# Optimization experiments

Hardware: AMD Instinct MI355X
Metric: run time of the kernel (lower is better)

Reference implementation:

```python
import jax, jax.numpy as jnp
import numpy as np

RNN_HID = 64
INPUT_DIM = 35
SEQ_LEN = 48
BATCH = 4096


def setup_inputs() -> dict:
    key = jax.random.key(0)
    ks = jax.random.split(key, 16)
    x_t = jax.random.normal(ks[0], (BATCH, SEQ_LEN, INPUT_DIM), jnp.float32)
    masks = (jax.random.uniform(ks[1], (BATCH, SEQ_LEN, INPUT_DIM)) > 0.2).astype(jnp.float32)
    deltas = jax.random.uniform(ks[2], (BATCH, SEQ_LEN, INPUT_DIM), jnp.float32)
    evals = jax.random.normal(ks[3], (BATCH, SEQ_LEN, INPUT_DIM), jnp.float32)
    eval_masks = (jax.random.uniform(ks[4], (BATCH, SEQ_LEN, INPUT_DIM)) > 0.8).astype(jnp.float32)
    is_train = jnp.ones((BATCH,), jnp.float32)

    in_sz = INPUT_DIM * 2  # LSTMCell input = concat(x_c, m)
    s_lstm = 1.0 / np.sqrt(RNN_HID)
    # torch LSTMCell params: W_ih [4H, in], W_hh [4H, H], b_ih [4H], b_hh [4H]
    W_ih = jax.random.uniform(ks[5], (4 * RNN_HID, in_sz), jnp.float32, -s_lstm, s_lstm)
    W_hh = jax.random.uniform(ks[6], (4 * RNN_HID, RNN_HID), jnp.float32, -s_lstm, s_lstm)
    b_ih = jax.random.uniform(ks[7], (4 * RNN_HID,), jnp.float32, -s_lstm, s_lstm)
    b_hh = jax.random.uniform(ks[8], (4 * RNN_HID,), jnp.float32, -s_lstm, s_lstm)
    W_reg = jax.random.uniform(ks[9], (INPUT_DIM, RNN_HID), jnp.float32, -s_lstm, s_lstm)
    b_reg = jax.random.uniform(ks[10], (INPUT_DIM,), jnp.float32, -s_lstm, s_lstm)
    # TemporalDecay: W [RNN_HID, input_dim], b [RNN_HID]
    W_td = jax.random.uniform(ks[11], (RNN_HID, INPUT_DIM), jnp.float32, -s_lstm, s_lstm)
    b_td = jax.random.uniform(ks[12], (RNN_HID,), jnp.float32, -s_lstm, s_lstm)
    # out Linear(RNN_HID -> 1)
    W_out = jax.random.uniform(ks[13], (1, RNN_HID), jnp.float32, -s_lstm, s_lstm)
    b_out = jax.random.uniform(ks[14], (1,), jnp.float32, -s_lstm, s_lstm)
    return {
        'x_t': x_t, 'masks': masks, 'deltas': deltas, 'evals': evals,
        'eval_masks': eval_masks, 'is_train': is_train,
        'W_ih': W_ih, 'W_hh': W_hh, 'b_ih': b_ih, 'b_hh': b_hh,
        'W_reg': W_reg, 'b_reg': b_reg, 'W_td': W_td, 'b_td': b_td,
        'W_out': W_out, 'b_out': b_out,
    }


def _lstm_cell(inp, h, c, W_ih, W_hh, b_ih, b_hh):
    # gates ordered i, f, g, o as in torch.nn.LSTMCell
    gates = inp @ W_ih.T + h @ W_hh.T + b_ih + b_hh  # [B, 4H]
    i, f, g, o = jnp.split(gates, 4, axis=-1)
    i = jax.nn.sigmoid(i)
    f = jax.nn.sigmoid(f)
    g = jnp.tanh(g)
    o = jax.nn.sigmoid(o)
    c_new = f * c + i * g
    h_new = o * jnp.tanh(c_new)
    return h_new, c_new


def reference(x_t, masks, deltas, evals, eval_masks, is_train,
              W_ih, W_hh, b_ih, b_hh, W_reg, b_reg, W_td, b_td, W_out, b_out):
    B, T, D = x_t.shape
    h0 = jnp.zeros((B, RNN_HID), x_t.dtype)
    c0 = jnp.zeros((B, RNN_HID), x_t.dtype)

    def step(carry, xs):
        h, c, x_loss = carry
        x, m, d = xs  # each [B, D]
        x_hat = h @ W_reg.T + b_reg
        x_c = m * x + (1.0 - m) * x_hat
        x_loss = x_loss + jnp.sum(jnp.abs(x - x_hat) * m) / (jnp.sum(m) + 1e-5)
        inputs = jnp.concatenate([x_c, m], axis=1)  # [B, 2D]
        # temporal decay (computed as in original, result unused)
        gamma = jnp.exp(-jax.nn.relu(d @ W_td.T + b_td))
        h, c = _lstm_cell(inputs, h, c, W_ih, W_hh, b_ih, b_hh)
        return (h, c, x_loss), x_c

    xs = (jnp.swapaxes(x_t, 0, 1), jnp.swapaxes(masks, 0, 1), jnp.swapaxes(deltas, 0, 1))
    (h, c, x_loss), imp = jax.lax.scan(step, (h0, c0, jnp.float32(0.0)), xs)
    imputations = jnp.swapaxes(imp, 0, 1)  # [B, T, D]
    y_h = jax.nn.sigmoid(h @ W_out.T + b_out)
    loss = x_loss / T  # y_loss == 0
    return loss, y_h, imputations
```

## Files before the change

kernel.cpp:

```cpp
#include <hip/hip_runtime.h>
#include <stdint.h>

#define B_    4096
#define T_    48
#define D_    35
#define KROW  168
#define ROWEL (T_ * D_)
#define L2E   1.44269504f

typedef float f32x4 __attribute__((ext_vector_type(4)));
typedef short bf16x8 __attribute__((ext_vector_type(8)));

static __device__ __forceinline__ uint32_t fbits(float x){union{float f;uint32_t u;}v;v.f=x;return v.u;}
static __device__ __forceinline__ float bitsf(uint32_t u){union{uint32_t u;float f;}v;v.u=u;return v.f;}
static __device__ __forceinline__ float bf2f(uint32_t b){return bitsf(b<<16);}
static __device__ __forceinline__ unsigned short f2bf_rne(float x){
    uint32_t u=fbits(x); return (unsigned short)((u+0x7fffu+((u>>16)&1u))>>16);
}
static __device__ __forceinline__ float rcp_(float x){return __builtin_amdgcn_rcpf(x);}
static __device__ __forceinline__ float exp2_(float x){return __builtin_amdgcn_exp2f(x);}
#define MFMA __builtin_amdgcn_mfma_f32_16x16x32_bf16

static __device__ __forceinline__ void step_barrier() {
    asm volatile("s_waitcnt lgkmcnt(0)" ::: "memory");
    __builtin_amdgcn_s_barrier();
    __builtin_amdgcn_sched_barrier(0);
}


__global__ __launch_bounds__(512, 1)
void brits_main(const float* __restrict__ x_t, const float* __restrict__ masks,
                const float* __restrict__ W_ih, const float* __restrict__ W_hh,
                const float* __restrict__ b_ih, const float* __restrict__ b_hh,
                const float* __restrict__ W_reg, const float* __restrict__ b_reg,
                const float* __restrict__ W_out, const float* __restrict__ b_out,
                float* __restrict__ ws, float* __restrict__ out)
{
    __shared__ __align__(16) unsigned short Abuf[2][16 * KROW];
    __shared__ __align__(16) unsigned short stash[16 * ROWEL];
    __shared__ unsigned long long mbits[16 * T_];
    __shared__ float lsum[T_ * 3 * 64];
    __shared__ float wout[65];

    const int tid    = threadIdx.x;
    const int lane   = tid & 63;
    const int w      = tid >> 6;
    const int g      = lane >> 4;
    const int cc     = lane & 15;
    const int batch0 = blockIdx.x * 16;
    const int u      = (w & 3) * 16 + cc;
    const int u2     = (w - 4) * 16 + cc;

    for (int i = tid; i < 16 * KROW; i += 512) ((uint32_t*)Abuf)[i] = 0;
    if (tid < 65) wout[tid] = (tid < 64) ? W_out[tid] : b_out[0];

    for (int i = tid; i < 16 * 210; i += 512) {
        const int r = i / 210;
        const int o = (i - r * 210) * 8;
        const float* xp = x_t   + (size_t)(batch0 + r) * ROWEL + o;
        const float* mp = masks + (size_t)(batch0 + r) * ROWEL + o;
        float xv[8], mv[8];
        *(float4*)&xv[0] = *(const float4*)xp; *(float4*)&xv[4] = *(const float4*)(xp + 4);
        *(float4*)&mv[0] = *(const float4*)mp; *(float4*)&mv[4] = *(const float4*)(mp + 4);
        unsigned short pk[8];
        #pragma unroll
        for (int k = 0; k < 8; ++k) pk[k] = f2bf_rne(mv[k] * xv[k]);
        *(uint4*)&stash[r * ROWEL + o] = *(const uint4*)pk;
    }
    for (int p = tid; p < 16 * T_; p += 512) {
        const int r = p / T_, t = p - r * T_;
        const float* mp = masks + (size_t)(batch0 + r) * ROWEL + t * D_;
        unsigned long long bits = 0;
        for (int d = 0; d < D_; ++d) bits |= (unsigned long long)(mp[d] != 0.f) << d;
        mbits[p] = bits;
    }

    bf16x8 Wf[4][5];
    float bIs = 0.f, bFs = 0.f, bGs = 0.f, bOs = 0.f;
    if (w < 4) {
        #pragma unroll
        for (int G = 0; G < 4; ++G) {
            const int n = G * 64 + u;
            #pragma unroll
            for (int kc = 0; kc < 5; ++kc) {
                bf16x8 v;
                #pragma unroll
                for (int i = 0; i < 8; ++i) {
                    const int k = kc * 32 + 8 * g + i;
                    float f = 0.f;
                    if (k < 70)                  f = W_ih[n * 70 + k];
                    else if (k >= 72 && k < 136) f = W_hh[n * 64 + (k - 72)];
                    v[i] = (short)f2bf_rne(f);
                }
                Wf[G][kc] = v;
            }
        }
        bIs = -(b_ih[u]       + b_hh[u])       * L2E;
        bFs = -(b_ih[64 + u]  + b_hh[64 + u])  * L2E;
        bGs = -(b_ih[128 + u] + b_hh[128 + u]) * 2.f * L2E;
        bOs = -(b_ih[192 + u] + b_hh[192 + u]) * L2E;
    }
    bf16x8 Wr0 = {0,0,0,0,0,0,0,0}, Wr1 = {0,0,0,0,0,0,0,0};
    float brg = 0.f;
    const bool pw = (w >= 4) && (w < 7);
    const bool pl = pw && (u2 < 35);
    if (pl) {
        #pragma unroll
        for (int i = 0; i < 8; ++i) {
            Wr0[i] = (short)f2bf_rne(W_reg[u2 * 64 + 8 * g + i]);
            Wr1[i] = (short)f2bf_rne(W_reg[u2 * 64 + 32 + 8 * g + i]);
        }
        brg = b_reg[u2];
    }
    __syncthreads();

    unsigned long long PM[4] = {0, 0, 0, 0};
    uint32_t xmr[4] = {0, 0, 0, 0};
    float* orow[4];
    if (pl) {
        #pragma unroll
        for (int j = 0; j < 4; ++j) {
            const int row = 4 * g + j;
            unsigned long long pm = 0;
            for (int t = 0; t < T_; ++t)
                pm |= ((mbits[row * T_ + t] >> u2) & 1ull) << t;
            PM[j] = pm;
            xmr[j] = stash[row * ROWEL + u2];
            Abuf[0][row * KROW + 35 + u2] = (pm & 1ull) ? (unsigned short)0x3F80 : (unsigned short)0;
            orow[j] = out + 1 + B_ + (size_t)(batch0 + row) * ROWEL + u2;
        }
    }
    __syncthreads();

    float c_[4] = {0.f, 0.f, 0.f, 0.f};

    for (int t = 0; t < T_; ++t) {
        unsigned short* A  = Abuf[t & 1];
        unsigned short* An = Abuf[(t + 1) & 1];

        f32x4 gIa = {0,0,0,0}, gFa = {0,0,0,0}, gGa = {0,0,0,0}, gOa = {0,0,0,0};
        f32x4 gIb = {0,0,0,0}, gFb = {0,0,0,0}, gGb = {0,0,0,0}, gOb = {0,0,0,0};

        if (w < 4) {
            bf16x8 a2 = *(const bf16x8*)&A[cc * KROW + 64  + 8 * g];
            bf16x8 a3 = *(const bf16x8*)&A[cc * KROW + 96  + 8 * g];
            bf16x8 a4 = *(const bf16x8*)&A[cc * KROW + 128 + 8 * g];
            gIa = MFMA(a2, Wf[0][2], gIa, 0,0,0);
            gFa = MFMA(a2, Wf[1][2], gFa, 0,0,0);
            gGa = MFMA(a2, Wf[2][2], gGa, 0,0,0);
            gOa = MFMA(a2, Wf[3][2], gOa, 0,0,0);
            gIb = MFMA(a3, Wf[0][3], gIb, 0,0,0);
            gFb = MFMA(a3, Wf[1][3], gFb, 0,0,0);
            gGb = MFMA(a3, Wf[2][3], gGb, 0,0,0);
            gOb = MFMA(a3, Wf[3][3], gOb, 0,0,0);
            gIa = MFMA(a4, Wf[0][4], gIa, 0,0,0);
            gFa = MFMA(a4, Wf[1][4], gFa, 0,0,0);
            gGa = MFMA(a4, Wf[2][4], gGa, 0,0,0);
            gOa = MFMA(a4, Wf[3][4], gOa, 0,0,0);
        } else if (pw) {
            bf16x8 ah0 = *(const bf16x8*)&A[cc * KROW + 72  + 8 * g];
            bf16x8 ah1 = *(const bf16x8*)&A[cc * KROW + 104 + 8 * g];
            f32x4 p0 = {0,0,0,0};
            p0 = MFMA(ah0, Wr0, p0, 0,0,0);
            p0 = MFMA(ah1, Wr1, p0, 0,0,0);
            float lnum = 0.f;
            if (pl) {
                #pragma unroll
                for (int j = 0; j < 4; ++j) {
                    const int row = 4 * g + j;
                    const float xh = p0[j] + brg;
                    const float xm = bf2f(xmr[j]);
                    const uint32_t mb = (uint32_t)(PM[j] >> t) & 1u;
                    lnum += mb ? fabsf(xm - xh) : 0.f;
                    const unsigned short xc16 = mb ? (unsigned short)xmr[j] : f2bf_rne(xh);
                    A[row * KROW + u2] = xc16;
                    An[row * KROW + 35 + u2] =
                        ((PM[j] >> (t + 1)) & 1ull) ? (unsigned short)0x3F80 : (unsigned short)0;
                    orow[j][t * D_] = bf2f((uint32_t)xc16);
                }
            }
            lsum[(t * 3 + (w - 4)) * 64 + lane] = lnum;
        }
        step_barrier();

        if (w < 4) {
            bf16x8 a0 = *(const bf16x8*)&A[cc * KROW + 0  + 8 * g];
            bf16x8 a1 = *(const bf16x8*)&A[cc * KROW + 32 + 8 * g];
            gIa = MFMA(a0, Wf[0][0], gIa, 0,0,0);
            gFa = MFMA(a0, Wf[1][0], gFa, 0,0,0);
            gGa = MFMA(a0, Wf[2][0], gGa, 0,0,0);
            gOa = MFMA(a0, Wf[3][0], gOa, 0,0,0);
            gIb = MFMA(a1, Wf[0][1], gIb, 0,0,0);
            gFb = MFMA(a1, Wf[1][1], gFb, 0,0,0);
            gGb = MFMA(a1, Wf[2][1], gGb, 0,0,0);
            gOb = MFMA(a1, Wf[3][1], gOb, 0,0,0);
            const f32x4 gI = gIa + gIb;
            const f32x4 gF = gFa + gFb;
            const f32x4 gG = gGa + gGb;
            const f32x4 gO = gOa + gOb;
            #pragma unroll
            for (int j = 0; j < 4; ++j) {
                const float iv = rcp_(1.f + exp2_(fmaf(gI[j], -L2E,       bIs)));
                const float fv = rcp_(1.f + exp2_(fmaf(gF[j], -L2E,       bFs)));
                const float gv = fmaf(2.f, rcp_(1.f + exp2_(fmaf(gG[j], -2.f * L2E, bGs))), -1.f);
                const float ov = rcp_(1.f + exp2_(fmaf(gO[j], -L2E,       bOs)));
                const float cn = fmaf(fv, c_[j], iv * gv);
                c_[j] = cn;
                const float th = fmaf(2.f, rcp_(1.f + exp2_(cn * (-2.f * L2E))), -1.f);
                An[(4 * g + j) * KROW + 72 + u] = (unsigned short)(fbits(ov * th) >> 16);
            }
        } else if (pl && t + 1 < T_) {
            #pragma unroll
            for (int j = 0; j < 4; ++j)
                xmr[j] = stash[(4 * g + j) * ROWEL + (t + 1) * D_ + u2];
        }
        step_barrier();
    }

    __syncthreads();

    if (tid < T_) {
        const int t = tid;
        float num = 0.f;
        for (int i = 0; i < 192; ++i) num += lsum[t * 192 + i];
        float den = 0.f;
        for (int r = 0; r < 16; ++r) den += (float)__popcll(mbits[r * T_ + t]);
        atomicAdd(&ws[t * 8 + (blockIdx.x & 7)], num);
        atomicAdd(&ws[(T_ + t) * 8 + (blockIdx.x & 7)], den);
    }

    if (w == 1) {
        float p = 0.f;
        #pragma unroll
        for (int k = 0; k < 16; ++k)
            p += bf2f(Abuf[0][cc * KROW + 72 + 16 * g + k]) * wout[16 * g + k];
        p += __shfl_xor(p, 16, 64);
        p += __shfl_xor(p, 32, 64);
        if (lane < 16) out[1 + batch0 + cc] = rcp_(1.f + exp2_(-(p + wout[64]) * L2E));
    }
}

__global__ void post_kernel(const float* __restrict__ ws, float* __restrict__ out)
{
    const int t = threadIdx.x;
    float v = 0.f;
    if (t < T_) {
        float num = 0.f, den = 0.f;
        #pragma unroll
        for (int s = 0; s < 8; ++s) {
            num += ws[t * 8 + s];
            den += ws[(T_ + t) * 8 + s];
        }
        v = num / (den + 1e-5f);
    }
    #pragma unroll
    for (int off = 1; off < 64; off <<= 1) v += __shfl_xor(v, off, 64);
    if (t == 0) out[0] = v * (1.0f / T_);
}

extern "C" void kernel_launch(void* const* d_in, const int* in_sizes, int n_in,
                              void* d_out, int out_size, void* d_ws, size_t ws_size,
                              hipStream_t stream) {
    const float* x_t   = (const float*)d_in[0];
    const float* masks = (const float*)d_in[1];
    const float* W_ih  = (const float*)d_in[6];
    const float* W_hh  = (const float*)d_in[7];
    const float* b_ih  = (const float*)d_in[8];
    const float* b_hh  = (const float*)d_in[9];
    const float* W_reg = (const float*)d_in[10];
    const float* b_reg = (const float*)d_in[11];
    const float* W_out = (const float*)d_in[14];
    const float* b_out = (const float*)d_in[15];
    float* out = (float*)d_out;
    float* ws  = (float*)d_ws;

    hipMemsetAsync(ws, 0, 2 * T_ * 8 * sizeof(float), stream);
    brits_main<<<B_ / 16, 512, 0, stream>>>(x_t, masks, W_ih, W_hh, b_ih, b_hh,
                                            W_reg, b_reg, W_out, b_out, ws, out);
    post_kernel<<<1, 64, 0, stream>>>(ws, out);
}
```

Measured before the change: 86.66 us.

## Stream x_t from global memory per step instead of staging a bf16 stash

Removes the up-front staging of masked x values into a large shared-memory bf16 stash. Each step instead reads x directly from global memory two steps ahead, using two alternating register buffers. The time loop is unrolled by two so the buffers stay in registers. Imputed outputs are now written as full fp32 values rather than bf16-rounded ones. This cuts the prologue load phase and frees shared memory, at the cost of strided global loads inside the serial recurrence, whose latency is meant to be hidden by the two-step prefetch.

```diff
diff --git a/kernel.cpp b/kernel.cpp
--- a/kernel.cpp
+++ b/kernel.cpp
@@ -13,12 +13,13 @@
 
 static __device__ __forceinline__ uint32_t fbits(float x){union{float f;uint32_t u;}v;v.f=x;return v.u;}
 static __device__ __forceinline__ float bitsf(uint32_t u){union{uint32_t u;float f;}v;v.u=u;return v.f;}
-static __device__ __forceinline__ float bf2f(uint32_t b){return bitsf(b<<16);}
+static __device__ __forceinline__ float bf2f(unsigned short b){return bitsf(((uint32_t)b)<<16);}
 static __device__ __forceinline__ unsigned short f2bf_rne(float x){
     uint32_t u=fbits(x); return (unsigned short)((u+0x7fffu+((u>>16)&1u))>>16);
 }
 static __device__ __forceinline__ float rcp_(float x){return __builtin_amdgcn_rcpf(x);}
 static __device__ __forceinline__ float exp2_(float x){return __builtin_amdgcn_exp2f(x);}
+
 #define MFMA __builtin_amdgcn_mfma_f32_16x16x32_bf16
 
 static __device__ __forceinline__ void step_barrier() {
@@ -37,7 +38,6 @@
                 float* __restrict__ ws, float* __restrict__ out)
 {
     __shared__ __align__(16) unsigned short Abuf[2][16 * KROW];
-    __shared__ __align__(16) unsigned short stash[16 * ROWEL];
     __shared__ unsigned long long mbits[16 * T_];
     __shared__ float lsum[T_ * 3 * 64];
     __shared__ float wout[65];
@@ -54,19 +54,6 @@
     for (int i = tid; i < 16 * KROW; i += 512) ((uint32_t*)Abuf)[i] = 0;
     if (tid < 65) wout[tid] = (tid < 64) ? W_out[tid] : b_out[0];
 
-    for (int i = tid; i < 16 * 210; i += 512) {
-        const int r = i / 210;
-        const int o = (i - r * 210) * 8;
-        const float* xp = x_t   + (size_t)(batch0 + r) * ROWEL + o;
-        const float* mp = masks + (size_t)(batch0 + r) * ROWEL + o;
-        float xv[8], mv[8];
-        *(float4*)&xv[0] = *(const float4*)xp; *(float4*)&xv[4] = *(const float4*)(xp + 4);
-        *(float4*)&mv[0] = *(const float4*)mp; *(float4*)&mv[4] = *(const float4*)(mp + 4);
-        unsigned short pk[8];
-        #pragma unroll
-        for (int k = 0; k < 8; ++k) pk[k] = f2bf_rne(mv[k] * xv[k]);
-        *(uint4*)&stash[r * ROWEL + o] = *(const uint4*)pk;
-    }
     for (int p = tid; p < 16 * T_; p += 512) {
         const int r = p / T_, t = p - r * T_;
         const float* mp = masks + (size_t)(batch0 + r) * ROWEL + t * D_;
@@ -115,8 +102,10 @@
     __syncthreads();
 
     unsigned long long PM[4] = {0, 0, 0, 0};
-    uint32_t xmr[4] = {0, 0, 0, 0};
+    const float* xrow[4];
     float* orow[4];
+    float xrA[4] = {0.f, 0.f, 0.f, 0.f};
+    float xrB[4] = {0.f, 0.f, 0.f, 0.f};
     if (pl) {
         #pragma unroll
         for (int j = 0; j < 4; ++j) {
@@ -125,16 +114,18 @@
             for (int t = 0; t < T_; ++t)
                 pm |= ((mbits[row * T_ + t] >> u2) & 1ull) << t;
             PM[j] = pm;
-            xmr[j] = stash[row * ROWEL + u2];
+            xrow[j] = x_t + (size_t)(batch0 + row) * ROWEL + u2;
+            orow[j] = out + 1 + B_ + (size_t)(batch0 + row) * ROWEL + u2;
+            xrA[j] = xrow[j][0];
+            xrB[j] = xrow[j][D_];
             Abuf[0][row * KROW + 35 + u2] = (pm & 1ull) ? (unsigned short)0x3F80 : (unsigned short)0;
-            orow[j] = out + 1 + B_ + (size_t)(batch0 + row) * ROWEL + u2;
         }
     }
     __syncthreads();
 
     float c_[4] = {0.f, 0.f, 0.f, 0.f};
 
-    for (int t = 0; t < T_; ++t) {
+    auto step = [&](int t, float (&xr)[4]) {
         unsigned short* A  = Abuf[t & 1];
         unsigned short* An = Abuf[(t + 1) & 1];
 
@@ -169,14 +160,14 @@
                 for (int j = 0; j < 4; ++j) {
                     const int row = 4 * g + j;
                     const float xh = p0[j] + brg;
-                    const float xm = bf2f(xmr[j]);
                     const uint32_t mb = (uint32_t)(PM[j] >> t) & 1u;
-                    lnum += mb ? fabsf(xm - xh) : 0.f;
-                    const unsigned short xc16 = mb ? (unsigned short)xmr[j] : f2bf_rne(xh);
-                    A[row * KROW + u2] = xc16;
+                    const float xv = xr[j];
+                    lnum += mb ? fabsf(xv - xh) : 0.f;
+                    const float xc = mb ? xv : xh;
+                    A[row * KROW + u2] = f2bf_rne(xc);
                     An[row * KROW + 35 + u2] =
                         ((PM[j] >> (t + 1)) & 1ull) ? (unsigned short)0x3F80 : (unsigned short)0;
-                    orow[j][t * D_] = bf2f((uint32_t)xc16);
+                    orow[j][t * D_] = xc;
                 }
             }
             lsum[(t * 3 + (w - 4)) * 64 + lane] = lnum;
@@ -209,12 +200,18 @@
                 const float th = fmaf(2.f, rcp_(1.f + exp2_(cn * (-2.f * L2E))), -1.f);
                 An[(4 * g + j) * KROW + 72 + u] = (unsigned short)(fbits(ov * th) >> 16);
             }
-        } else if (pl && t + 1 < T_) {
+        } else if (pl && t + 2 < T_) {
             #pragma unroll
             for (int j = 0; j < 4; ++j)
-                xmr[j] = stash[(4 * g + j) * ROWEL + (t + 1) * D_ + u2];
+                xr[j] = xrow[j][(t + 2) * D_];
         }
         step_barrier();
+    };
+
+    #pragma unroll 1
+    for (int tt = 0; tt < T_ / 2; ++tt) {
+        step(2 * tt,     xrA);
+        step(2 * tt + 1, xrB);
     }
 
     __syncthreads();
```

Measured after the change: 78.08 us. -9.9%, faster.
